# Performance work log

Hardware: AMD Instinct MI355X
Metric: run time of the kernel (lower is better)

Reference implementation:

```python
import jax, jax.numpy as jnp
import numpy as np

B, S, D, H = 256, 128, 2, 512


def _lstm_cell(x, h, c, Wih, Whh, bih, bhh):
    # PyTorch LSTMCell gate order: i, f, g, o
    z = x @ Wih.T + bih + h @ Whh.T + bhh
    i, f, g, o = jnp.split(z, 4, axis=-1)
    c_new = jax.nn.sigmoid(f) * c + jax.nn.sigmoid(i) * jnp.tanh(g)
    h_new = jax.nn.sigmoid(o) * jnp.tanh(c_new)
    return h_new, c_new


def setup_inputs() -> dict:
    key = jax.random.key(0)
    ks = jax.random.split(key, 16)
    sc = 0.05
    inp = {
        "x": jax.random.uniform(ks[0], (B, S, D), dtype=jnp.float32),
        "enc_Wih": jax.random.normal(ks[1], (4 * H, D), dtype=jnp.float32) * sc,
        "enc_Whh": jax.random.normal(ks[2], (4 * H, H), dtype=jnp.float32) * sc,
        "enc_bih": jax.random.normal(ks[3], (4 * H,), dtype=jnp.float32) * sc,
        "enc_bhh": jax.random.normal(ks[4], (4 * H,), dtype=jnp.float32) * sc,
        "dec_Wih": jax.random.normal(ks[5], (4 * H, H), dtype=jnp.float32) * sc,
        "dec_Whh": jax.random.normal(ks[6], (4 * H, H), dtype=jnp.float32) * sc,
        "dec_bih": jax.random.normal(ks[7], (4 * H,), dtype=jnp.float32) * sc,
        "dec_bhh": jax.random.normal(ks[8], (4 * H,), dtype=jnp.float32) * sc,
        "W1": jax.random.normal(ks[9], (H, H), dtype=jnp.float32) * sc,
        "b1": jax.random.normal(ks[10], (H,), dtype=jnp.float32) * sc,
        "W2": jax.random.normal(ks[11], (H, H), dtype=jnp.float32) * sc,
        "b2": jax.random.normal(ks[12], (H,), dtype=jnp.float32) * sc,
        "v": jax.random.normal(ks[13], (1, H), dtype=jnp.float32) * sc,
        "bv": jax.random.normal(ks[14], (1,), dtype=jnp.float32) * sc,
    }
    return inp


def reference(x, enc_Wih, enc_Whh, enc_bih, enc_bhh,
              dec_Wih, dec_Whh, dec_bih, dec_bhh,
              W1, b1, W2, b2, v, bv):
    # ---- encoder: LSTMCell scan over sequence ----
    def enc_step(carry, xt):
        h, c = carry
        h, c = _lstm_cell(xt, h, c, enc_Wih, enc_Whh, enc_bih, enc_bhh)
        return (h, c), h

    h0 = jnp.zeros((B, H), dtype=x.dtype)
    c0 = jnp.zeros((B, H), dtype=x.dtype)
    (h_enc, c_enc), enc_hs = jax.lax.scan(enc_step, (h0, c0),
                                          jnp.transpose(x, (1, 0, 2)))
    enc_hs = jnp.transpose(enc_hs, (1, 0, 2))          # [B, S, H]
    W1e = enc_hs @ W1.T + b1                            # [B, S, H]

    # ---- decoder with per-step additive attention ----
    dec_in = jnp.full((B, H), -1.0, dtype=x.dtype)      # constant decoder input

    def dec_step(carry, _):
        h, c = carry
        h, c = _lstm_cell(dec_in, h, c, dec_Wih, dec_Whh, dec_bih, dec_bhh)
        W2h = h @ W2.T + b2                             # [B, H]
        u = jnp.tanh(W1e + W2h[:, None, :]) @ v[0] + bv[0]  # [B, S]
        a = jax.nn.softmax(u, axis=1)                   # [B, S]
        h_new = jnp.einsum('bs,bsh->bh', a, enc_hs)     # attention glimpse
        return (h_new, c), a

    _, attn = jax.lax.scan(dec_step, (h_enc, c_enc), None, length=S)
    return jnp.transpose(attn, (1, 0, 2))               # [B, S, S]
```

## Files before the change

### kernel.cpp

```cpp
#include <hip/hip_runtime.h>
#include <hip/hip_fp16.h>

#define B_ 256
#define S_ 128
#define D_ 2
#define H_ 512
#define NBLK 256

struct alignas(16) H8 { __half2 h[4]; };

__device__ __forceinline__ float sigm(float x){ return 1.f/(1.f+__expf(-x)); }
__device__ __forceinline__ float tanh_(float x){ return 1.f - 2.f/(__expf(2.f*x)+1.f); }

__device__ __forceinline__ float ldc(const float* p){
    return __hip_atomic_load(p, __ATOMIC_RELAXED, __HIP_MEMORY_SCOPE_AGENT);
}
__device__ __forceinline__ void stc(float* p, float v){
    __hip_atomic_store(p, v, __ATOMIC_RELAXED, __HIP_MEMORY_SCOPE_AGENT);
}
__device__ __forceinline__ unsigned ldu(const unsigned* p){
    return __hip_atomic_load(p, __ATOMIC_RELAXED, __HIP_MEMORY_SCOPE_AGENT);
}
__device__ __forceinline__ void stu(unsigned* p, unsigned v){
    __hip_atomic_store(p, v, __ATOMIC_RELAXED, __HIP_MEMORY_SCOPE_AGENT);
}

__device__ __forceinline__ void gbar(unsigned* bar){
    __syncthreads();
    if (threadIdx.x == 0) {
        asm volatile("s_waitcnt vmcnt(0)" ::: "memory");
        const int grp = blockIdx.x >> 4;
        unsigned* gc = bar + grp * 16;
        unsigned* gg = bar + 256 + grp * 16;
        unsigned* rc = bar + 512;
        unsigned* rg = bar + 528;
        unsigned gen = ldu(gg);
        if (__hip_atomic_fetch_add(gc, 1u, __ATOMIC_RELAXED, __HIP_MEMORY_SCOPE_AGENT) == 15u) {
            stu(gc, 0u);
            unsigned rgen = ldu(rg);
            if (__hip_atomic_fetch_add(rc, 1u, __ATOMIC_RELAXED, __HIP_MEMORY_SCOPE_AGENT) == 15u) {
                stu(rc, 0u);
                stu(rg, rgen + 1u);
            } else {
                while (ldu(rg) == rgen) __builtin_amdgcn_s_sleep(1);
            }
            stu(gg, gen + 1u);
        } else {
            while (ldu(gg) == gen) __builtin_amdgcn_s_sleep(1);
        }
    }
    __syncthreads();
}

__device__ __forceinline__ void stage32(float (*Hs)[H_], const float* src,
                                        size_t str, int b0, int tid){
    float r[32];
#pragma unroll
    for (int i = 0; i < 32; i++) r[i] = ldc(src + (size_t)(b0 + i) * str + tid);
#pragma unroll
    for (int i = 0; i < 32; i++) Hs[i][tid] = r[i];
}

__global__ __launch_bounds__(256) void prep6(
    const float* __restrict__ dWih, const float* __restrict__ dbih,
    const float* __restrict__ dbhh, const float* __restrict__ ebih,
    const float* __restrict__ ebhh, float* __restrict__ dxw,
    float* __restrict__ ebias)
{
    int j = blockIdx.x * 256 + threadIdx.x;
    const float* row = dWih + (size_t)j * H_;
    float s = 0.f;
    for (int k = 0; k < H_; k++) s += row[k];
    dxw[j]   = dbih[j] + dbhh[j] - s;
    ebias[j] = ebih[j] + ebhh[j];
}

__global__ __launch_bounds__(256) void pack_whh(
    const float* __restrict__ eW, const float* __restrict__ dW,
    float* __restrict__ pe, float* __restrict__ pd)
{
    size_t n = (size_t)blockIdx.x * 256 + threadIdx.x;
    int sel = (int)(n >> 20);
    int m = (int)(n & 1048575);
    int c = m & 3, rw = (m >> 2) & 63, i4 = (m >> 8) & 15;
    int ks = (m >> 12) & 7, jt = m >> 15;
    int g = rw >> 4, hu = rw & 15;
    size_t src = (size_t)(g * H_ + jt * 16 + hu) * H_ + ks * 64 + i4 * 4 + c;
    if (sel) pd[m] = dW[src]; else pe[m] = eW[src];
}

__device__ __forceinline__ void load_w64(const float* Wsrc, int packed,
                                         int jt, int ks, int rw, float* w)
{
    if (packed) {
        const float4* wp = (const float4*)Wsrc + (size_t)(jt * 8 + ks) * 1024 + rw;
#pragma unroll
        for (int i = 0; i < 16; i++) {
            float4 t4 = wp[(size_t)i * 64];
            w[4*i]=t4.x; w[4*i+1]=t4.y; w[4*i+2]=t4.z; w[4*i+3]=t4.w;
        }
    } else {
        int g = rw >> 4, hu = rw & 15;
        const float4* wp = (const float4*)(Wsrc + (size_t)(g * H_ + jt*16 + hu) * H_ + ks * 64);
#pragma unroll
        for (int i = 0; i < 16; i++) {
            float4 t4 = wp[i];
            w[4*i]=t4.x; w[4*i+1]=t4.y; w[4*i+2]=t4.z; w[4*i+3]=t4.w;
        }
    }
}

__global__ __launch_bounds__(512, 1) void enc_p(
    const float* __restrict__ x, const float* __restrict__ eWih,
    const float* __restrict__ Wsrc, int packed,
    const float* __restrict__ ebias, float* __restrict__ enc_hs,
    __half* __restrict__ eh16, float* __restrict__ c_fin, unsigned* bar)
{
    __shared__ float smem[16384];
    float (*Hs)[H_]    = (float (*)[H_])smem;
    float (*P)[32][64] = (float (*)[32][64])smem;

    const int tid = threadIdx.x;
    const int ks = tid >> 6, rw = tid & 63;
    const int bt = blockIdx.x >> 5, jt = blockIdx.x & 31;
    const int b0 = bt * 32, hu0 = jt * 16;

    float w[64];
    load_w64(Wsrc, packed, jt, ks, rw, w);

    const int fb = tid >> 4, fh = tid & 15;
    const int fhu = hu0 + fh;
    float eb4[4], wi0[4], wi1[4];
#pragma unroll
    for (int g = 0; g < 4; g++) {
        eb4[g] = ebias[g*H_ + fhu];
        wi0[g] = eWih[(size_t)(g*H_ + fhu)*D_ + 0];
        wi1[g] = eWih[(size_t)(g*H_ + fhu)*D_ + 1];
    }
    float creg = 0.f;

    for (int t = 0; t < S_; t++) {
        float acc[32];
        if (t == 0) {
#pragma unroll
            for (int b = 0; b < 32; b++) acc[b] = 0.f;
        } else {
            stage32(Hs, enc_hs + (size_t)(t - 1) * H_, (size_t)S_ * H_, b0, tid);
            __syncthreads();
#pragma unroll 2
            for (int b = 0; b < 32; b++) {
                const float4* hp = (const float4*)&Hs[b][ks * 64];
                float s = 0.f;
#pragma unroll
                for (int i = 0; i < 16; i++) {
                    float4 h4 = hp[i];
                    s += h4.x*w[4*i] + h4.y*w[4*i+1] + h4.z*w[4*i+2] + h4.w*w[4*i+3];
                }
                acc[b] = s;
            }
            __syncthreads();
        }
#pragma unroll
        for (int b = 0; b < 32; b++) P[ks][b][rw ^ ((b & 3) << 4)] = acc[b];
        __syncthreads();
        {
            float z[4];
#pragma unroll
            for (int g = 0; g < 4; g++) {
                int row = g*16 + fh;
                float s2 = 0.f;
#pragma unroll
                for (int k8 = 0; k8 < 8; k8++)
                    s2 += P[k8][fb][row ^ ((fb & 3) << 4)];
                z[g] = s2 + eb4[g];
            }
            int bb = b0 + fb;
            float x0 = x[((size_t)bb*S_ + t)*D_ + 0];
            float x1 = x[((size_t)bb*S_ + t)*D_ + 1];
#pragma unroll
            for (int g = 0; g < 4; g++) z[g] += x0*wi0[g] + x1*wi1[g];
            float cn = sigm(z[1])*creg + sigm(z[0])*tanh_(z[2]);
            float hn = sigm(z[3])*tanh_(cn);
            creg = cn;
            stc(&enc_hs[((size_t)bb*S_ + t)*H_ + fhu], hn);
            if (eh16) eh16[((size_t)bb*S_ + t)*H_ + fhu] = __float2half(hn);
        }
        if (t < S_ - 1) gbar(bar);
    }
    stc(&c_fin[(size_t)(b0 + fb)*H_ + fhu], creg);
}

template<int BM, int BN, int TM, int TN, typename OT>
__global__ __launch_bounds__((BM/TM)*(BN/TN)) void gemm_bias(
    const float* __restrict__ A, const float* __restrict__ Bm,
    const float* __restrict__ bias, OT* __restrict__ C,
    int M, int N, int K)
{
    constexpr int BK = 32;
    constexpr int TH = (BM / TM) * (BN / TN);
    constexpr int AL = BM * BK / TH;
    constexpr int BL = BN * BK / TH;
    constexpr int RP = TH / BK;
    __shared__ float As[BK][BM + 4];
    __shared__ float Bs[BK][BN + 4];
    const int tid = threadIdx.x;
    const int tn = tid % (BN / TN);
    const int tm = tid / (BN / TN);
    const int m0 = blockIdx.x * BM, n0 = blockIdx.y * BN;
    const int lk = tid % BK, lr = tid / BK;

    float acc[TM][TN];
#pragma unroll
    for (int i = 0; i < TM; i++)
#pragma unroll
        for (int j = 0; j < TN; j++) acc[i][j] = 0.f;

    float areg[AL], breg[BL];
#pragma unroll
    for (int i = 0; i < AL; i++) areg[i] = A[(size_t)(m0 + lr + i * RP) * K + lk];
#pragma unroll
    for (int i = 0; i < BL; i++) breg[i] = Bm[(size_t)(n0 + lr + i * RP) * K + lk];

    const int NC = K / BK;
    for (int c = 0; c < NC; c++) {
        __syncthreads();
#pragma unroll
        for (int i = 0; i < AL; i++) As[lk][lr + i * RP] = areg[i];
#pragma unroll
        for (int i = 0; i < BL; i++) Bs[lk][lr + i * RP] = breg[i];
        __syncthreads();
        if (c + 1 < NC) {
            int k0 = (c + 1) * BK;
#pragma unroll
            for (int i = 0; i < AL; i++) areg[i] = A[(size_t)(m0 + lr + i * RP) * K + k0 + lk];
#pragma unroll
            for (int i = 0; i < BL; i++) breg[i] = Bm[(size_t)(n0 + lr + i * RP) * K + k0 + lk];
        }
#pragma unroll
        for (int k = 0; k < BK; k++) {
            float av[TM], bvv[TN];
#pragma unroll
            for (int i = 0; i < TM; i++) av[i] = As[k][tm * TM + i];
#pragma unroll
            for (int j = 0; j < TN; j++) bvv[j] = Bs[k][tn * TN + j];
#pragma unroll
            for (int i = 0; i < TM; i++)
#pragma unroll
                for (int j = 0; j < TN; j++) acc[i][j] += av[i] * bvv[j];
        }
    }
#pragma unroll
    for (int i = 0; i < TM; i++) {
        int m = m0 + tm * TM + i;
#pragma unroll
        for (int j = 0; j < TN; j++) {
            int n = n0 + tn * TN + j;
            C[(size_t)m * N + n] = (OT)(acc[i][j] + bias[n]);
        }
    }
}

__global__ __launch_bounds__(512, 1) void dec_p(
    const float* __restrict__ Wsrc, int packed,
    const float* __restrict__ dxw,
    const float* __restrict__ W2, const float* __restrict__ b2,
    const float* __restrict__ vv, const float* __restrict__ bv,
    const float* __restrict__ enc_hs, const __half* __restrict__ W1e16,
    const __half* __restrict__ eb16, const float* __restrict__ c_fin,
    float* __restrict__ h_dec, float* __restrict__ w2h,
    float* __restrict__ h_glim, float* __restrict__ out,
    unsigned* bar)
{
    __shared__ float smem[16384];
    float (*Hs)[H_]     = (float (*)[H_])smem;
    float (*P)[32][64]  = (float (*)[32][64])smem;
    float (*P2)[32][16] = (float (*)[32][16])smem;
    float* qq  = smem;
    float* ua  = smem + 512;
    float* red = smem + 640;
    float* P3  = smem + 1024;

    const int tid = threadIdx.x;
    const int ks = tid >> 6, rw = tid & 63;
    const int bt = blockIdx.x >> 5, jt = blockIdx.x & 31;
    const int b0 = bt * 32, hu0 = jt * 16;
    const int ln = tid & 63, wv = tid >> 6;

    float w[64];
    load_w64(Wsrc, packed, jt, ks, rw, w);

    const int rsub = (tid >> 4) & 3, jj = tid & 15;
    float w2r[16];
    {
        const float4* p4 = (const float4*)(W2 + (size_t)(hu0 + jj)*H_ + ks*64 + rsub*16);
#pragma unroll
        for (int i = 0; i < 4; i++) {
            float4 t4 = p4[i];
            w2r[4*i]=t4.x; w2r[4*i+1]=t4.y; w2r[4*i+2]=t4.z; w2r[4*i+3]=t4.w;
        }
    }

    const int fb = tid >> 4, fh = tid & 15;
    const int fhu = hu0 + fh;
    float db4[4];
#pragma unroll
    for (int g = 0; g < 4; g++) db4[g] = dxw[g*H_ + fhu];
    const float b2f = b2[fhu];
    float creg = c_fin[(size_t)(b0 + fb)*H_ + fhu];

    const int ab = blockIdx.x;
    const __half* w1b = W1e16 + (size_t)ab * S_ * H_;
    const __half* ebh = eb16 ? (eb16 + (size_t)ab * S_ * H_) : (const __half*)nullptr;
    const float* ebf = enc_hs + (size_t)ab * S_ * H_;
    const float4 vr0 = *(const float4*)(vv + ln*8);
    const float4 vr1 = *(const float4*)(vv + ln*8 + 4);
    const float bvr = bv[0];

    for (int t = 0; t < S_; t++) {
        {
            const float* hsrc = (t == 0) ? (enc_hs + (size_t)(S_-1)*H_) : h_glim;
            const size_t hstr = (t == 0) ? (size_t)(S_*H_) : (size_t)H_;
            stage32(Hs, hsrc, hstr, b0, tid);
            __syncthreads();
            float acc[32];
#pragma unroll 2
            for (int b = 0; b < 32; b++) {
                const float4* hp = (const float4*)&Hs[b][ks * 64];
                float s = 0.f;
#pragma unroll
                for (int i = 0; i < 16; i++) {
                    float4 h4 = hp[i];
                    s += h4.x*w[4*i] + h4.y*w[4*i+1] + h4.z*w[4*i+2] + h4.w*w[4*i+3];
                }
                acc[b] = s;
            }
            __syncthreads();
#pragma unroll
            for (int b = 0; b < 32; b++) P[ks][b][rw ^ ((b & 3) << 4)] = acc[b];
            __syncthreads();
            float z[4];
#pragma unroll
            for (int g = 0; g < 4; g++) {
                int row = g*16 + fh;
                float s2 = 0.f;
#pragma unroll
                for (int k8 = 0; k8 < 8; k8++)
                    s2 += P[k8][fb][row ^ ((fb & 3) << 4)];
                z[g] = s2 + db4[g];
            }
            float cn = sigm(z[1])*creg + sigm(z[0])*tanh_(z[2]);
            float hn = sigm(z[3])*tanh_(cn);
            creg = cn;
            stc(&h_dec[(size_t)(b0 + fb)*H_ + fhu], hn);
        }
        gbar(bar);
        {
            stage32(Hs, h_dec, (size_t)H_, b0, tid);
            __syncthreads();
            float a2[32];
#pragma unroll 2
            for (int b = 0; b < 32; b++) {
                const float4* hp = (const float4*)&Hs[b][ks*64 + rsub*16];
                float s = 0.f;
#pragma unroll
                for (int i = 0; i < 4; i++) {
                    float4 h4 = hp[i];
                    s += h4.x*w2r[4*i] + h4.y*w2r[4*i+1] + h4.z*w2r[4*i+2] + h4.w*w2r[4*i+3];
                }
                a2[b] = s;
            }
            __syncthreads();
#pragma unroll
            for (int b = 0; b < 32; b++) P2[b][ks*4 + rsub][jj] = a2[b];
            __syncthreads();
            float s2 = 0.f;
#pragma unroll
            for (int p = 0; p < 32; p++) s2 += P2[fb][p][fh];
            stc(&w2h[(size_t)(b0 + fb)*H_ + fhu], s2 + b2f);
        }
        gbar(bar);
        {
            qq[tid] = ldc(&w2h[(size_t)ab*H_ + tid]);
            __syncthreads();
            float4 q0 = *(float4*)&qq[ln*8];
            float4 q1 = *(float4*)&qq[ln*8 + 4];
#pragma unroll 4
            for (int si = 0; si < 16; si++) {
                int s = wv*16 + si;
                H8 w8 = *(const H8*)(w1b + (size_t)s*H_ + ln*8);
                float2 a0 = __half22float2(w8.h[0]);
                float2 a1 = __half22float2(w8.h[1]);
                float2 a2 = __half22float2(w8.h[2]);
                float2 a3 = __half22float2(w8.h[3]);
                float sum = tanh_(a0.x+q0.x)*vr0.x + tanh_(a0.y+q0.y)*vr0.y
                          + tanh_(a1.x+q0.z)*vr0.z + tanh_(a1.y+q0.w)*vr0.w
                          + tanh_(a2.x+q1.x)*vr1.x + tanh_(a2.y+q1.y)*vr1.y
                          + tanh_(a3.x+q1.z)*vr1.z + tanh_(a3.y+q1.w)*vr1.w;
#pragma unroll
                for (int off = 32; off; off >>= 1) sum += __shfl_xor(sum, off);
                if (ln == 0) ua[s] = sum + bvr;
            }
            __syncthreads();
            float e = 0.f;
            if (tid < 128) {
                float m = ua[tid];
#pragma unroll
                for (int off = 32; off; off >>= 1) m = fmaxf(m, __shfl_xor(m, off));
                if (ln == 0) red[tid >> 6] = m;
            }
            __syncthreads();
            if (tid < 128) {
                float mx = fmaxf(red[0], red[1]);
                e = __expf(ua[tid] - mx);
                float ss = e;
#pragma unroll
                for (int off = 32; off; off >>= 1) ss += __shfl_xor(ss, off);
                if (ln == 0) red[2 + (tid >> 6)] = ss;
            }
            __syncthreads();
            if (tid < 128) {
                float a = e / (red[2] + red[3]);
                ua[tid] = a;
                out[(size_t)ab*S_*S_ + (size_t)t*S_ + tid] = a;
            }
            __syncthreads();
            float acc8[8];
#pragma unroll
            for (int i = 0; i < 8; i++) acc8[i] = 0.f;
            if (ebh) {
#pragma unroll 4
                for (int si = 0; si < 16; si++) {
                    int s = wv*16 + si;
                    H8 e8 = *(const H8*)(ebh + (size_t)s*H_ + ln*8);
                    float a = ua[s];
                    float2 p0 = __half22float2(e8.h[0]);
                    float2 p1 = __half22float2(e8.h[1]);
                    float2 p2 = __half22float2(e8.h[2]);
                    float2 p3 = __half22float2(e8.h[3]);
                    acc8[0] += a*p0.x; acc8[1] += a*p0.y;
                    acc8[2] += a*p1.x; acc8[3] += a*p1.y;
                    acc8[4] += a*p2.x; acc8[5] += a*p2.y;
                    acc8[6] += a*p3.x; acc8[7] += a*p3.y;
                }
            } else {
#pragma unroll 4
                for (int si = 0; si < 16; si++) {
                    int s = wv*16 + si;
                    const float4* ep = (const float4*)(ebf + (size_t)s*H_ + ln*8);
                    float4 e0 = ep[0], e1 = ep[1];
                    float a = ua[s];
                    acc8[0] += a*e0.x; acc8[1] += a*e0.y;
                    acc8[2] += a*e0.z; acc8[3] += a*e0.w;
                    acc8[4] += a*e1.x; acc8[5] += a*e1.y;
                    acc8[6] += a*e1.z; acc8[7] += a*e1.w;
                }
            }
#pragma unroll
            for (int i = 0; i < 8; i++) P3[wv*576 + ln*9 + i] = acc8[i];
            __syncthreads();
            {
                float g = 0.f;
                int base = (tid >> 3) * 9 + (tid & 7);
#pragma unroll
                for (int w8 = 0; w8 < 8; w8++) g += P3[w8*576 + base];
                stc(&h_glim[(size_t)ab*H_ + tid], g);
            }
        }
        if (t < S_ - 1) gbar(bar);
    }
}

extern "C" void kernel_launch(void* const* d_in, const int* in_sizes, int n_in,
                              void* d_out, int out_size, void* d_ws, size_t ws_size,
                              hipStream_t stream)
{
    const float* x    = (const float*)d_in[0];
    const float* eWih = (const float*)d_in[1];
    const float* eWhh = (const float*)d_in[2];
    const float* ebih = (const float*)d_in[3];
    const float* ebhh = (const float*)d_in[4];
    const float* dWih = (const float*)d_in[5];
    const float* dWhh = (const float*)d_in[6];
    const float* dbih = (const float*)d_in[7];
    const float* dbhh = (const float*)d_in[8];
    const float* W1   = (const float*)d_in[9];
    const float* b1   = (const float*)d_in[10];
    const float* W2   = (const float*)d_in[11];
    const float* b2   = (const float*)d_in[12];
    const float* vv   = (const float*)d_in[13];
    const float* bv   = (const float*)d_in[14];
    float* out = (float*)d_out;

    float* ws      = (float*)d_ws;
    float* enc_hs  = ws;
    float* h_dec   = enc_hs + (size_t)B_ * S_ * H_;
    float* h_glim  = h_dec  + (size_t)B_ * H_;
    float* w2h     = h_glim + (size_t)B_ * H_;
    float* c_fin   = w2h    + (size_t)B_ * H_;
    float* dxw     = c_fin  + (size_t)B_ * H_;
    float* ebias   = dxw    + 2048;
    unsigned* bars = (unsigned*)(ebias + 2048);
    __half* W1e16  = (__half*)(ebias + 2048 + 2048);
    float* after16 = (float*)(W1e16) + 8388608;
    __half* eh16   = (__half*)after16;
    float* wpk_e   = after16 + 8388608;
    float* wpk_d   = wpk_e + 1048576;

    size_t mand_f   = (size_t)(after16 - ws);
    int have_eh16 = (ws_size >= (mand_f + 8388608u) * sizeof(float)) ? 1 : 0;
    int packed    = (ws_size >= (mand_f + 8388608u + 2097152u) * sizeof(float)) ? 1 : 0;
    if (!have_eh16) eh16 = nullptr;

    hipMemsetAsync(bars, 0, 2048 * sizeof(unsigned), stream);
    prep6<<<8, 256, 0, stream>>>(dWih, dbih, dbhh, ebih, ebhh, dxw, ebias);
    if (packed)
        pack_whh<<<8192, 256, 0, stream>>>(eWhh, dWhh, wpk_e, wpk_d);

    const float* We = packed ? wpk_e : eWhh;
    const float* Wd = packed ? wpk_d : dWhh;

    enc_p<<<NBLK, 512, 0, stream>>>(x, eWih, We, packed, ebias, enc_hs, eh16, c_fin, bars);

    gemm_bias<128, 128, 8, 8, __half>
        <<<dim3((B_ * S_) / 128, H_ / 128), 256, 0, stream>>>(
        enc_hs, W1, b1, W1e16, B_ * S_, H_, H_);

    dec_p<<<NBLK, 512, 0, stream>>>(Wd, packed, dxw, W2, b2, vv, bv,
                                    enc_hs, W1e16, eh16, c_fin,
                                    h_dec, w2h, h_glim, out, bars + 1024);
}
```

Before: 11.92 ms.

## Split decoder gate/W2 matvec into two half-batches and cache W1e in registers

The persistent decoder kernel now stages the 32-row hidden batch in two 16-row halves, writing partial sums to two separate shared-memory regions. This halves the accumulator arrays and the staging register footprint. Each block's slice of W1e (fp16) is also loaded once into registers before the time loop instead of being reread from global memory every step. The trade-offs are extra __syncthreads per phase, the final reduction running on only 256 of 512 threads, and 64 more VGPRs held for W1e, which may cause spills.

```diff
diff --git a/kernel.cpp b/kernel.cpp
--- a/kernel.cpp
+++ b/kernel.cpp
@@ -60,6 +60,14 @@
 #pragma unroll
     for (int i = 0; i < 32; i++) Hs[i][tid] = r[i];
 }
+__device__ __forceinline__ void stage16(float (*Hs)[H_], const float* src,
+                                        size_t str, int b0, int tid){
+    float r[16];
+#pragma unroll
+    for (int i = 0; i < 16; i++) r[i] = ldc(src + (size_t)(b0 + i) * str + tid);
+#pragma unroll
+    for (int i = 0; i < 16; i++) Hs[i][tid] = r[i];
+}
 
 __global__ __launch_bounds__(256) void prep6(
     const float* __restrict__ dWih, const float* __restrict__ dbih,
@@ -272,9 +280,11 @@
     unsigned* bar)
 {
     __shared__ float smem[16384];
-    float (*Hs)[H_]     = (float (*)[H_])smem;
-    float (*P)[32][64]  = (float (*)[32][64])smem;
-    float (*P2)[32][16] = (float (*)[32][16])smem;
+    float (*HsA)[H_]    = (float (*)[H_])smem;
+    float (*P0)[16][64] = (float (*)[16][64])(smem + 8192);
+    float (*P1)[16][64] = (float (*)[16][64])smem;
+    float (*Q0)[32][16] = (float (*)[32][16])(smem + 8192);
+    float (*Q1)[32][16] = (float (*)[32][16])smem;
     float* qq  = smem;
     float* ua  = smem + 512;
     float* red = smem + 640;
@@ -316,16 +326,21 @@
     const float4 vr1 = *(const float4*)(vv + ln*8 + 4);
     const float bvr = bv[0];
 
+    H8 w1r[16];
+#pragma unroll
+    for (int si = 0; si < 16; si++)
+        w1r[si] = *(const H8*)(w1b + (size_t)(wv*16 + si)*H_ + ln*8);
+
     for (int t = 0; t < S_; t++) {
         {
             const float* hsrc = (t == 0) ? (enc_hs + (size_t)(S_-1)*H_) : h_glim;
             const size_t hstr = (t == 0) ? (size_t)(S_*H_) : (size_t)H_;
-            stage32(Hs, hsrc, hstr, b0, tid);
-            __syncthreads();
-            float acc[32];
+            float acc[16];
+            stage16(HsA, hsrc, hstr, b0, tid);
+            __syncthreads();
 #pragma unroll 2
-            for (int b = 0; b < 32; b++) {
-                const float4* hp = (const float4*)&Hs[b][ks * 64];
+            for (int b = 0; b < 16; b++) {
+                const float4* hp = (const float4*)&HsA[b][ks * 64];
                 float s = 0.f;
 #pragma unroll
                 for (int i = 0; i < 16; i++) {
@@ -336,31 +351,52 @@
             }
             __syncthreads();
 #pragma unroll
-            for (int b = 0; b < 32; b++) P[ks][b][rw ^ ((b & 3) << 4)] = acc[b];
-            __syncthreads();
-            float z[4];
-#pragma unroll
-            for (int g = 0; g < 4; g++) {
-                int row = g*16 + fh;
-                float s2 = 0.f;
-#pragma unroll
-                for (int k8 = 0; k8 < 8; k8++)
-                    s2 += P[k8][fb][row ^ ((fb & 3) << 4)];
-                z[g] = s2 + db4[g];
-            }
-            float cn = sigm(z[1])*creg + sigm(z[0])*tanh_(z[2]);
-            float hn = sigm(z[3])*tanh_(cn);
-            creg = cn;
-            stc(&h_dec[(size_t)(b0 + fb)*H_ + fhu], hn);
+            for (int b = 0; b < 16; b++) P0[ks][b][rw ^ ((b & 3) << 4)] = acc[b];
+            stage16(HsA, hsrc, hstr, b0 + 16, tid);
+            __syncthreads();
+#pragma unroll 2
+            for (int b = 0; b < 16; b++) {
+                const float4* hp = (const float4*)&HsA[b][ks * 64];
+                float s = 0.f;
+#pragma unroll
+                for (int i = 0; i < 16; i++) {
+                    float4 h4 = hp[i];
+                    s += h4.x*w[4*i] + h4.y*w[4*i+1] + h4.z*w[4*i+2] + h4.w*w[4*i+3];
+                }
+                acc[b] = s;
+            }
+            __syncthreads();
+#pragma unroll
+            for (int b = 0; b < 16; b++) P1[ks][b][rw ^ ((b & 3) << 4)] = acc[b];
+            __syncthreads();
+            if (tid < 256) {
+                float (*Pf)[16][64] = (fb < 16) ? P0 : P1;
+                const int bl = fb & 15;
+                float z[4];
+#pragma unroll
+                for (int g = 0; g < 4; g++) {
+                    int row = g*16 + fh;
+                    float s2 = 0.f;
+#pragma unroll
+                    for (int k8 = 0; k8 < 8; k8++)
+                        s2 += Pf[k8][bl][row ^ ((bl & 3) << 4)];
+                    z[g] = s2 + db4[g];
+                }
+                float cn = sigm(z[1])*creg + sigm(z[0])*tanh_(z[2]);
+                float hn = sigm(z[3])*tanh_(cn);
+                creg = cn;
+                stc(&h_dec[(size_t)(b0 + fb)*H_ + fhu], hn);
+            }
         }
         gbar(bar);
         {
-            stage32(Hs, h_dec, (size_t)H_, b0, tid);
-            __syncthreads();
-            float a2[32];
+            const int kk = ks * 64 + rsub * 16;
+            float a2[16];
+            stage16(HsA, h_dec, (size_t)H_, b0, tid);
+            __syncthreads();
 #pragma unroll 2
-            for (int b = 0; b < 32; b++) {
-                const float4* hp = (const float4*)&Hs[b][ks*64 + rsub*16];
+            for (int b = 0; b < 16; b++) {
+                const float4* hp = (const float4*)&HsA[b][kk];
                 float s = 0.f;
 #pragma unroll
                 for (int i = 0; i < 4; i++) {
@@ -371,12 +407,32 @@
             }
             __syncthreads();
 #pragma unroll
-            for (int b = 0; b < 32; b++) P2[b][ks*4 + rsub][jj] = a2[b];
-            __syncthreads();
-            float s2 = 0.f;
-#pragma unroll
-            for (int p = 0; p < 32; p++) s2 += P2[fb][p][fh];
-            stc(&w2h[(size_t)(b0 + fb)*H_ + fhu], s2 + b2f);
+            for (int b = 0; b < 16; b++) Q0[b][ks*4 + rsub][jj] = a2[b];
+            stage16(HsA, h_dec, (size_t)H_, b0 + 16, tid);
+            __syncthreads();
+#pragma unroll 2
+            for (int b = 0; b < 16; b++) {
+                const float4* hp = (const float4*)&HsA[b][kk];
+                float s = 0.f;
+#pragma unroll
+                for (int i = 0; i < 4; i++) {
+                    float4 h4 = hp[i];
+                    s += h4.x*w2r[4*i] + h4.y*w2r[4*i+1] + h4.z*w2r[4*i+2] + h4.w*w2r[4*i+3];
+                }
+                a2[b] = s;
+            }
+            __syncthreads();
+#pragma unroll
+            for (int b = 0; b < 16; b++) Q1[b][ks*4 + rsub][jj] = a2[b];
+            __syncthreads();
+            if (tid < 256) {
+                float (*Qf)[32][16] = (fb < 16) ? Q0 : Q1;
+                const int bl = fb & 15;
+                float s2 = 0.f;
+#pragma unroll
+                for (int p = 0; p < 32; p++) s2 += Qf[bl][p][fh];
+                stc(&w2h[(size_t)(b0 + fb)*H_ + fhu], s2 + b2f);
+            }
         }
         gbar(bar);
         {
@@ -384,14 +440,13 @@
             __syncthreads();
             float4 q0 = *(float4*)&qq[ln*8];
             float4 q1 = *(float4*)&qq[ln*8 + 4];
-#pragma unroll 4
+#pragma unroll
             for (int si = 0; si < 16; si++) {
                 int s = wv*16 + si;
-                H8 w8 = *(const H8*)(w1b + (size_t)s*H_ + ln*8);
-                float2 a0 = __half22float2(w8.h[0]);
-                float2 a1 = __half22float2(w8.h[1]);
-                float2 a2 = __half22float2(w8.h[2]);
-                float2 a3 = __half22float2(w8.h[3]);
+                float2 a0 = __half22float2(w1r[si].h[0]);
+                float2 a1 = __half22float2(w1r[si].h[1]);
+                float2 a2 = __half22float2(w1r[si].h[2]);
+                float2 a3 = __half22float2(w1r[si].h[3]);
                 float sum = tanh_(a0.x+q0.x)*vr0.x + tanh_(a0.y+q0.y)*vr0.y
                           + tanh_(a1.x+q0.z)*vr0.z + tanh_(a1.y+q0.w)*vr0.w
                           + tanh_(a2.x+q1.x)*vr1.x + tanh_(a2.y+q1.y)*vr1.y
```

New measurement: 15.19 ms. 27.4% more time.

## Replace two-level grid barrier with per-group barriers and cache W1e in LDS

Applied to the files above, without the earlier changes.

The global two-level barrier becomes a barrier over groups of 32 blocks, since each batch group of 32 rows only depends on its own 32 blocks. The decoder now copies its per-batch W1e half-precision slice (128 KB) into dynamic shared memory once, instead of rereading it from global memory every step. Encoder and decoder staging is split into two 16-row halves to keep shared usage small, and the encoder-hidden loads are issued early to hide latency. The risks are that 160 KB of dynamic LDS may not fit or launch, and the extra half-loop syncs add cost.

```diff
diff --git a/kernel.cpp b/kernel.cpp
--- a/kernel.cpp
+++ b/kernel.cpp
@@ -6,6 +6,7 @@
 #define D_ 2
 #define H_ 512
 #define NBLK 256
+#define GRP 32
 
 struct alignas(16) H8 { __half2 h[4]; };
 
@@ -25,40 +26,22 @@
     __hip_atomic_store(p, v, __ATOMIC_RELAXED, __HIP_MEMORY_SCOPE_AGENT);
 }
 
-__device__ __forceinline__ void gbar(unsigned* bar){
+__device__ __forceinline__ void gbar32(unsigned* base, int grp){
     __syncthreads();
     if (threadIdx.x == 0) {
+        unsigned* c = base + grp * 32;
+        unsigned* g = base + grp * 32 + 16;
         asm volatile("s_waitcnt vmcnt(0)" ::: "memory");
-        const int grp = blockIdx.x >> 4;
-        unsigned* gc = bar + grp * 16;
-        unsigned* gg = bar + 256 + grp * 16;
-        unsigned* rc = bar + 512;
-        unsigned* rg = bar + 528;
-        unsigned gen = ldu(gg);
-        if (__hip_atomic_fetch_add(gc, 1u, __ATOMIC_RELAXED, __HIP_MEMORY_SCOPE_AGENT) == 15u) {
-            stu(gc, 0u);
-            unsigned rgen = ldu(rg);
-            if (__hip_atomic_fetch_add(rc, 1u, __ATOMIC_RELAXED, __HIP_MEMORY_SCOPE_AGENT) == 15u) {
-                stu(rc, 0u);
-                stu(rg, rgen + 1u);
-            } else {
-                while (ldu(rg) == rgen) __builtin_amdgcn_s_sleep(1);
-            }
-            stu(gg, gen + 1u);
+        unsigned gen = ldu(g);
+        if (__hip_atomic_fetch_add(c, 1u, __ATOMIC_RELAXED, __HIP_MEMORY_SCOPE_AGENT) == GRP - 1u) {
+            stu(c, 0u);
+            asm volatile("s_waitcnt vmcnt(0)" ::: "memory");
+            stu(g, gen + 1u);
         } else {
-            while (ldu(gg) == gen) __builtin_amdgcn_s_sleep(1);
+            while (ldu(g) == gen) __builtin_amdgcn_s_sleep(1);
         }
     }
     __syncthreads();
-}
-
-__device__ __forceinline__ void stage32(float (*Hs)[H_], const float* src,
-                                        size_t str, int b0, int tid){
-    float r[32];
-#pragma unroll
-    for (int i = 0; i < 32; i++) r[i] = ldc(src + (size_t)(b0 + i) * str + tid);
-#pragma unroll
-    for (int i = 0; i < 32; i++) Hs[i][tid] = r[i];
 }
 
 __global__ __launch_bounds__(256) void prep6(
@@ -116,14 +99,14 @@
     const float* __restrict__ ebias, float* __restrict__ enc_hs,
     __half* __restrict__ eh16, float* __restrict__ c_fin, unsigned* bar)
 {
-    __shared__ float smem[16384];
-    float (*Hs)[H_]    = (float (*)[H_])smem;
-    float (*P)[32][64] = (float (*)[32][64])smem;
+    __shared__ float work[8192];
+    float (*Hs)[H_]    = (float (*)[H_])work;
+    float (*P)[16][64] = (float (*)[16][64])work;
 
     const int tid = threadIdx.x;
     const int ks = tid >> 6, rw = tid & 63;
-    const int bt = blockIdx.x >> 5, jt = blockIdx.x & 31;
-    const int b0 = bt * 32, hu0 = jt * 16;
+    const int grp = blockIdx.x >> 5, jt = blockIdx.x & 31;
+    const int b0 = grp * GRP, hu0 = jt * 16;
 
     float w[64];
     load_w64(Wsrc, packed, jt, ks, rw, w);
@@ -137,57 +120,73 @@
         wi0[g] = eWih[(size_t)(g*H_ + fhu)*D_ + 0];
         wi1[g] = eWih[(size_t)(g*H_ + fhu)*D_ + 1];
     }
-    float creg = 0.f;
+    float creg0 = 0.f, creg1 = 0.f;
 
     for (int t = 0; t < S_; t++) {
-        float acc[32];
-        if (t == 0) {
-#pragma unroll
-            for (int b = 0; b < 32; b++) acc[b] = 0.f;
-        } else {
-            stage32(Hs, enc_hs + (size_t)(t - 1) * H_, (size_t)S_ * H_, b0, tid);
-            __syncthreads();
+#pragma unroll 1
+        for (int hf = 0; hf < 2; hf++) {
+            float acc[16];
+            if (t == 0) {
+#pragma unroll
+                for (int b = 0; b < 16; b++) acc[b] = 0.f;
+            } else {
+                {
+                    float r[16];
+                    const float* src = enc_hs + (size_t)(t - 1) * H_;
+#pragma unroll
+                    for (int i = 0; i < 16; i++)
+                        r[i] = ldc(src + (size_t)(b0 + hf*16 + i) * (S_*H_) + tid);
+#pragma unroll
+                    for (int i = 0; i < 16; i++) Hs[i][tid] = r[i];
+                }
+                __syncthreads();
 #pragma unroll 2
-            for (int b = 0; b < 32; b++) {
-                const float4* hp = (const float4*)&Hs[b][ks * 64];
-                float s = 0.f;
-#pragma unroll
-                for (int i = 0; i < 16; i++) {
-                    float4 h4 = hp[i];
-                    s += h4.x*w[4*i] + h4.y*w[4*i+1] + h4.z*w[4*i+2] + h4.w*w[4*i+3];
-                }
-                acc[b] = s;
-            }
-            __syncthreads();
-        }
-#pragma unroll
-        for (int b = 0; b < 32; b++) P[ks][b][rw ^ ((b & 3) << 4)] = acc[b];
-        __syncthreads();
-        {
-            float z[4];
-#pragma unroll
-            for (int g = 0; g < 4; g++) {
-                int row = g*16 + fh;
-                float s2 = 0.f;
-#pragma unroll
-                for (int k8 = 0; k8 < 8; k8++)
-                    s2 += P[k8][fb][row ^ ((fb & 3) << 4)];
-                z[g] = s2 + eb4[g];
-            }
-            int bb = b0 + fb;
-            float x0 = x[((size_t)bb*S_ + t)*D_ + 0];
-            float x1 = x[((size_t)bb*S_ + t)*D_ + 1];
-#pragma unroll
-            for (int g = 0; g < 4; g++) z[g] += x0*wi0[g] + x1*wi1[g];
-            float cn = sigm(z[1])*creg + sigm(z[0])*tanh_(z[2]);
-            float hn = sigm(z[3])*tanh_(cn);
-            creg = cn;
-            stc(&enc_hs[((size_t)bb*S_ + t)*H_ + fhu], hn);
-            if (eh16) eh16[((size_t)bb*S_ + t)*H_ + fhu] = __float2half(hn);
-        }
-        if (t < S_ - 1) gbar(bar);
-    }
-    stc(&c_fin[(size_t)(b0 + fb)*H_ + fhu], creg);
+                for (int b = 0; b < 16; b++) {
+                    const float4* hp = (const float4*)&Hs[b][ks * 64];
+                    float s = 0.f;
+#pragma unroll
+                    for (int i = 0; i < 16; i++) {
+                        float4 h4 = hp[i];
+                        s += h4.x*w[4*i] + h4.y*w[4*i+1] + h4.z*w[4*i+2] + h4.w*w[4*i+3];
+                    }
+                    acc[b] = s;
+                }
+                __syncthreads();
+            }
+#pragma unroll
+            for (int b = 0; b < 16; b++) P[ks][b][rw ^ ((b & 3) << 4)] = acc[b];
+            __syncthreads();
+            if (tid < 256) {
+                float z[4];
+#pragma unroll
+                for (int g = 0; g < 4; g++) {
+                    int row = g*16 + fh;
+                    float s2 = 0.f;
+#pragma unroll
+                    for (int k8 = 0; k8 < 8; k8++)
+                        s2 += P[k8][fb][row ^ ((fb & 3) << 4)];
+                    z[g] = s2 + eb4[g];
+                }
+                int bb = b0 + hf*16 + fb;
+                float x0 = x[((size_t)bb*S_ + t)*D_ + 0];
+                float x1 = x[((size_t)bb*S_ + t)*D_ + 1];
+#pragma unroll
+                for (int g = 0; g < 4; g++) z[g] += x0*wi0[g] + x1*wi1[g];
+                float cold = hf ? creg1 : creg0;
+                float cn = sigm(z[1])*cold + sigm(z[0])*tanh_(z[2]);
+                float hn = sigm(z[3])*tanh_(cn);
+                if (hf) creg1 = cn; else creg0 = cn;
+                stc(&enc_hs[((size_t)bb*S_ + t)*H_ + fhu], hn);
+                if (eh16) eh16[((size_t)bb*S_ + t)*H_ + fhu] = __float2half(hn);
+            }
+            __syncthreads();
+        }
+        if (t < S_ - 1) gbar32(bar, grp);
+    }
+    if (tid < 256) {
+        stc(&c_fin[(size_t)(b0 + fb)*H_ + fhu],      creg0);
+        stc(&c_fin[(size_t)(b0 + 16 + fb)*H_ + fhu], creg1);
+    }
 }
 
 template<int BM, int BN, int TM, int TN, typename OT>
@@ -271,19 +270,22 @@
     float* __restrict__ h_glim, float* __restrict__ out,
     unsigned* bar)
 {
-    __shared__ float smem[16384];
-    float (*Hs)[H_]     = (float (*)[H_])smem;
-    float (*P)[32][64]  = (float (*)[32][64])smem;
-    float (*P2)[32][16] = (float (*)[32][16])smem;
-    float* qq  = smem;
-    float* ua  = smem + 512;
-    float* red = smem + 640;
-    float* P3  = smem + 1024;
+    extern __shared__ char smem_raw[];
+    __half* w1l = (__half*)smem_raw;
+    float* work = (float*)(smem_raw + 131072);
+    float (*Hs)[H_]     = (float (*)[H_])work;
+    float (*P)[16][64]  = (float (*)[16][64])work;
+    float (*Q)[32][16]  = (float (*)[32][16])work;
+    float* qq  = work;
+    float* ua  = work + 512;
+    float* red = work + 640;
+    float* P3  = work + 1024;
 
     const int tid = threadIdx.x;
     const int ks = tid >> 6, rw = tid & 63;
-    const int bt = blockIdx.x >> 5, jt = blockIdx.x & 31;
-    const int b0 = bt * 32, hu0 = jt * 16;
+    const int ab = blockIdx.x;
+    const int grp = ab >> 5, jt = ab & 31;
+    const int b0 = grp * GRP, hu0 = jt * 16;
     const int ln = tid & 63, wv = tid >> 6;
 
     float w[64];
@@ -306,88 +308,129 @@
 #pragma unroll
     for (int g = 0; g < 4; g++) db4[g] = dxw[g*H_ + fhu];
     const float b2f = b2[fhu];
-    float creg = c_fin[(size_t)(b0 + fb)*H_ + fhu];
-
-    const int ab = blockIdx.x;
-    const __half* w1b = W1e16 + (size_t)ab * S_ * H_;
+    float creg0 = c_fin[(size_t)(b0 + (fb & 15))*H_ + fhu];
+    float creg1 = c_fin[(size_t)(b0 + 16 + (fb & 15))*H_ + fhu];
+
     const __half* ebh = eb16 ? (eb16 + (size_t)ab * S_ * H_) : (const __half*)nullptr;
     const float* ebf = enc_hs + (size_t)ab * S_ * H_;
     const float4 vr0 = *(const float4*)(vv + ln*8);
     const float4 vr1 = *(const float4*)(vv + ln*8 + 4);
     const float bvr = bv[0];
 
+    {
+        const H8* src = (const H8*)(W1e16 + (size_t)ab * S_ * H_);
+        H8* dst = (H8*)w1l;
+#pragma unroll
+        for (int i = 0; i < 16; i++) dst[tid + i * 512] = src[tid + i * 512];
+    }
+    __syncthreads();
+
     for (int t = 0; t < S_; t++) {
         {
             const float* hsrc = (t == 0) ? (enc_hs + (size_t)(S_-1)*H_) : h_glim;
             const size_t hstr = (t == 0) ? (size_t)(S_*H_) : (size_t)H_;
-            stage32(Hs, hsrc, hstr, b0, tid);
-            __syncthreads();
-            float acc[32];
+#pragma unroll 1
+            for (int hf = 0; hf < 2; hf++) {
+                {
+                    float r[16];
+#pragma unroll
+                    for (int i = 0; i < 16; i++)
+                        r[i] = ldc(hsrc + (size_t)(b0 + hf*16 + i) * hstr + tid);
+#pragma unroll
+                    for (int i = 0; i < 16; i++) Hs[i][tid] = r[i];
+                }
+                __syncthreads();
+                float acc[16];
 #pragma unroll 2
-            for (int b = 0; b < 32; b++) {
-                const float4* hp = (const float4*)&Hs[b][ks * 64];
-                float s = 0.f;
-#pragma unroll
-                for (int i = 0; i < 16; i++) {
-                    float4 h4 = hp[i];
-                    s += h4.x*w[4*i] + h4.y*w[4*i+1] + h4.z*w[4*i+2] + h4.w*w[4*i+3];
-                }
-                acc[b] = s;
-            }
-            __syncthreads();
-#pragma unroll
-            for (int b = 0; b < 32; b++) P[ks][b][rw ^ ((b & 3) << 4)] = acc[b];
-            __syncthreads();
-            float z[4];
-#pragma unroll
-            for (int g = 0; g < 4; g++) {
-                int row = g*16 + fh;
-                float s2 = 0.f;
-#pragma unroll
-                for (int k8 = 0; k8 < 8; k8++)
-                    s2 += P[k8][fb][row ^ ((fb & 3) << 4)];
-                z[g] = s2 + db4[g];
-            }
-            float cn = sigm(z[1])*creg + sigm(z[0])*tanh_(z[2]);
-            float hn = sigm(z[3])*tanh_(cn);
-            creg = cn;
-            stc(&h_dec[(size_t)(b0 + fb)*H_ + fhu], hn);
-        }
-        gbar(bar);
+                for (int b = 0; b < 16; b++) {
+                    const float4* hp = (const float4*)&Hs[b][ks * 64];
+                    float s = 0.f;
+#pragma unroll
+                    for (int i = 0; i < 16; i++) {
+                        float4 h4 = hp[i];
+                        s += h4.x*w[4*i] + h4.y*w[4*i+1] + h4.z*w[4*i+2] + h4.w*w[4*i+3];
+                    }
+                    acc[b] = s;
+                }
+                __syncthreads();
+#pragma unroll
+                for (int b = 0; b < 16; b++) P[ks][b][rw ^ ((b & 3) << 4)] = acc[b];
+                __syncthreads();
+                if (tid < 256) {
+                    float z[4];
+#pragma unroll
+                    for (int g = 0; g < 4; g++) {
+                        int row = g*16 + fh;
+                        float s2 = 0.f;
+#pragma unroll
+                        for (int k8 = 0; k8 < 8; k8++)
+                            s2 += P[k8][fb][row ^ ((fb & 3) << 4)];
+                        z[g] = s2 + db4[g];
+                    }
+                    float cold = hf ? creg1 : creg0;
+                    float cn = sigm(z[1])*cold + sigm(z[0])*tanh_(z[2]);
+                    float hn = sigm(z[3])*tanh_(cn);
+                    if (hf) creg1 = cn; else creg0 = cn;
+                    stc(&h_dec[(size_t)(b0 + hf*16 + fb)*H_ + fhu], hn);
+                }
+                __syncthreads();
+            }
+        }
+        gbar32(bar, grp);
         {
-            stage32(Hs, h_dec, (size_t)H_, b0, tid);
-            __syncthreads();
-            float a2[32];
+            const int kk = ks * 64 + rsub * 16;
+#pragma unroll 1
+            for (int hf = 0; hf < 2; hf++) {
+                {
+                    float r[16];
+#pragma unroll
+                    for (int i = 0; i < 16; i++)
+                        r[i] = ldc(h_dec + (size_t)(b0 + hf*16 + i) * H_ + tid);
+#pragma unroll
+                    for (int i = 0; i < 16; i++) Hs[i][tid] = r[i];
+                }
+                __syncthreads();
+                float a2[16];
 #pragma unroll 2
-            for (int b = 0; b < 32; b++) {
-                const float4* hp = (const float4*)&Hs[b][ks*64 + rsub*16];
-                float s = 0.f;
-#pragma unroll
-                for (int i = 0; i < 4; i++) {
-                    float4 h4 = hp[i];
-                    s += h4.x*w2r[4*i] + h4.y*w2r[4*i+1] + h4.z*w2r[4*i+2] + h4.w*w2r[4*i+3];
-                }
-                a2[b] = s;
-            }
-            __syncthreads();
-#pragma unroll
-            for (int b = 0; b < 32; b++) P2[b][ks*4 + rsub][jj] = a2[b];
-            __syncthreads();
-            float s2 = 0.f;
-#pragma unroll
-            for (int p = 0; p < 32; p++) s2 += P2[fb][p][fh];
-            stc(&w2h[(size_t)(b0 + fb)*H_ + fhu], s2 + b2f);
-        }
-        gbar(bar);
+                for (int b = 0; b < 16; b++) {
+                    const float4* hp = (const float4*)&Hs[b][kk];
+                    float s = 0.f;
+#pragma unroll
+                    for (int i = 0; i < 4; i++) {
+                        float4 h4 = hp[i];
+                        s += h4.x*w2r[4*i] + h4.y*w2r[4*i+1] + h4.z*w2r[4*i+2] + h4.w*w2r[4*i+3];
+                    }
+                    a2[b] = s;
+                }
+                __syncthreads();
+#pragma unroll
+                for (int b = 0; b < 16; b++) Q[b][ks*4 + rsub][jj] = a2[b];
+                __syncthreads();
+                if (tid < 256) {
+                    float s2 = 0.f;
+#pragma unroll
+                    for (int p = 0; p < 32; p++) s2 += Q[fb][p][fh];
+                    stc(&w2h[(size_t)(b0 + hf*16 + fb)*H_ + fhu], s2 + b2f);
+                }
+                __syncthreads();
+            }
+        }
+        gbar32(bar, grp);
         {
             qq[tid] = ldc(&w2h[(size_t)ab*H_ + tid]);
+            H8 e8[16];
+            if (ebh) {
+#pragma unroll
+                for (int si = 0; si < 16; si++)
+                    e8[si] = *(const H8*)(ebh + (size_t)(wv*16 + si)*H_ + ln*8);
+            }
             __syncthreads();
             float4 q0 = *(float4*)&qq[ln*8];
             float4 q1 = *(float4*)&qq[ln*8 + 4];
-#pragma unroll 4
+#pragma unroll
             for (int si = 0; si < 16; si++) {
                 int s = wv*16 + si;
-                H8 w8 = *(const H8*)(w1b + (size_t)s*H_ + ln*8);
+                H8 w8 = *(const H8*)&w1l[(size_t)s*H_ + ln*8];
                 float2 a0 = __half22float2(w8.h[0]);
                 float2 a1 = __half22float2(w8.h[1]);
                 float2 a2 = __half22float2(w8.h[2]);
@@ -428,15 +471,14 @@
 #pragma unroll
             for (int i = 0; i < 8; i++) acc8[i] = 0.f;
             if (ebh) {
-#pragma unroll 4
+#pragma unroll
                 for (int si = 0; si < 16; si++) {
                     int s = wv*16 + si;
-                    H8 e8 = *(const H8*)(ebh + (size_t)s*H_ + ln*8);
                     float a = ua[s];
-                    float2 p0 = __half22float2(e8.h[0]);
-                    float2 p1 = __half22float2(e8.h[1]);
-                    float2 p2 = __half22float2(e8.h[2]);
-                    float2 p3 = __half22float2(e8.h[3]);
+                    float2 p0 = __half22float2(e8[si].h[0]);
+                    float2 p1 = __half22float2(e8[si].h[1]);
+                    float2 p2 = __half22float2(e8[si].h[2]);
+                    float2 p3 = __half22float2(e8[si].h[3]);
                     acc8[0] += a*p0.x; acc8[1] += a*p0.y;
                     acc8[2] += a*p1.x; acc8[3] += a*p1.y;
                     acc8[4] += a*p2.x; acc8[5] += a*p2.y;
@@ -466,7 +508,7 @@
                 stc(&h_glim[(size_t)ab*H_ + tid], g);
             }
         }
-        if (t < S_ - 1) gbar(bar);
+        if (t < S_ - 1) gbar32(bar, grp);
     }
 }
 
@@ -500,7 +542,7 @@
     float* dxw     = c_fin  + (size_t)B_ * H_;
     float* ebias   = dxw    + 2048;
     unsigned* bars = (unsigned*)(ebias + 2048);
-    __half* W1e16  = (__half*)(ebias + 2048 + 2048);
+    __half* W1e16  = (__half*)(ebias + 2048 + 1024);
     float* after16 = (float*)(W1e16) + 8388608;
     __half* eh16   = (__half*)after16;
     float* wpk_e   = after16 + 8388608;
@@ -511,7 +553,7 @@
     int packed    = (ws_size >= (mand_f + 8388608u + 2097152u) * sizeof(float)) ? 1 : 0;
     if (!have_eh16) eh16 = nullptr;
 
-    hipMemsetAsync(bars, 0, 2048 * sizeof(unsigned), stream);
+    hipMemsetAsync(bars, 0, 1024 * sizeof(unsigned), stream);
     prep6<<<8, 256, 0, stream>>>(dWih, dbih, dbhh, ebih, ebhh, dxw, ebias);
     if (packed)
         pack_whh<<<8192, 256, 0, stream>>>(eWhh, dWhh, wpk_e, wpk_d);
@@ -519,13 +561,14 @@
     const float* We = packed ? wpk_e : eWhh;
     const float* Wd = packed ? wpk_d : dWhh;
 
-    enc_p<<<NBLK, 512, 0, stream>>>(x, eWih, We, packed, ebias, enc_hs, eh16, c_fin, bars);
+    enc_p<<<NBLK, 512, 0, stream>>>(x, eWih, We, packed, ebias, enc_hs, eh16,
+                                    c_fin, bars);
 
     gemm_bias<128, 128, 8, 8, __half>
         <<<dim3((B_ * S_) / 128, H_ / 128), 256, 0, stream>>>(
         enc_hs, W1, b1, W1e16, B_ * S_, H_, H_);
 
-    dec_p<<<NBLK, 512, 0, stream>>>(Wd, packed, dxw, W2, b2, vv, bv,
-                                    enc_hs, W1e16, eh16, c_fin,
-                                    h_dec, w2h, h_glim, out, bars + 1024);
-}
+    dec_p<<<NBLK, 512, 163840, stream>>>(Wd, packed, dxw, W2, b2, vv, bv,
+                                         enc_hs, W1e16, eh16, c_fin,
+                                         h_dec, w2h, h_glim, out, bars + 512);
+}
```

Result: slower. 13.78 ms (+15.6%).
